# Kernel tuning notes

Measured on AMD Instinct MI355X. Metric: run time of the kernel, lower is better.

Reference implementation:

```python
import jax, jax.numpy as jnp
import numpy as np

QUERY_DIM = 1024
KEY_DIM = 1024
NUM_HEADS = 16
HEAD_DIM = QUERY_DIM // NUM_HEADS


def setup_inputs() -> dict:
    key = jax.random.key(0)
    ks = jax.random.split(key, 12)
    B, Sq, Sk = 2, 1024, 4096

    def xavier(k, fan_in, fan_out):
        limit = np.sqrt(6.0 / (fan_in + fan_out))
        return jax.random.uniform(k, (fan_in, fan_out), jnp.float32, -limit, limit)

    return {
        "query": jax.random.normal(ks[0], (B, Sq, QUERY_DIM), jnp.float32),
        "key": jax.random.normal(ks[1], (B, Sk, KEY_DIM), jnp.float32),
        "value": jax.random.normal(ks[2], (B, Sk, KEY_DIM), jnp.float32),
        "key_mask": jax.random.randint(ks[3], (B, Sk), 0, 2, jnp.int32),
        # projection weights stored as [in, out] for x @ W
        "Wq": xavier(ks[4], QUERY_DIM, NUM_HEADS * HEAD_DIM),
        "bq": jnp.zeros((NUM_HEADS * HEAD_DIM,), jnp.float32),
        "Wk": xavier(ks[5], KEY_DIM, NUM_HEADS * HEAD_DIM),
        "bk": jnp.zeros((NUM_HEADS * HEAD_DIM,), jnp.float32),
        "Wv": xavier(ks[6], KEY_DIM, NUM_HEADS * HEAD_DIM),
        "bv": jnp.zeros((NUM_HEADS * HEAD_DIM,), jnp.float32),
        "Wo": xavier(ks[7], NUM_HEADS * HEAD_DIM, QUERY_DIM),
        "bo": jnp.zeros((QUERY_DIM,), jnp.float32),
    }


def reference(query, key, value, key_mask, Wq, bq, Wk, bk, Wv, bv, Wo, bo):
    B, Sq, _ = query.shape
    Sk = key.shape[1]
    H, D = NUM_HEADS, HEAD_DIM
    scale = 1.0 / np.sqrt(D)

    q = (query @ Wq + bq).reshape(B, Sq, H, D)   # [B,Sq,H,D]
    k = (key @ Wk + bk).reshape(B, Sk, H, D)     # [B,Sk,H,D]
    v = (value @ Wv + bv).reshape(B, Sk, H, D)

    # scores: [B,H,Sq,Sk]
    scores = jnp.einsum("bqhd,bkhd->bhqk", q, k) * scale
    mask = (key_mask == 0)[:, None, None, :]  # [B,1,1,Sk]
    scores = jnp.where(mask, jnp.float32(-1e9), scores)
    probs = jax.nn.softmax(scores, axis=-1)
    # dropout is identity at eval (p effectively 0)
    ctx = jnp.einsum("bhqk,bkhd->bqhd", probs, v).reshape(B, Sq, H * D)
    return ctx @ Wo + bo
```

## Files before the change

### kernel.cpp

```cpp
#include <hip/hip_runtime.h>
#include <stdint.h>

#define NH 16
#define HD 64
#define SQ 1024
#define SK 4096
#define DM 1024
#define MQ 2048
#define MK 8192
#define MTOT 18432

typedef short s16x8 __attribute__((ext_vector_type(8)));
typedef float f32x4 __attribute__((ext_vector_type(4)));

#define GLOAD_LDS16(g, l) __builtin_amdgcn_global_load_lds( \
    (const __attribute__((address_space(1))) void*)(g), \
    (__attribute__((address_space(3))) void*)(l), 16, 0, 0)

__device__ __forceinline__ short f2bf(float f) {
  union { float f; uint32_t u; } v; v.f = f;
  uint32_t r = (v.u + 0x7FFFu + ((v.u >> 16) & 1u)) >> 16;
  return (short)(uint16_t)r;
}
__device__ __forceinline__ short f2bf_rz(float f) {
  union { float f; uint32_t u; } v; v.f = f;
  return (short)(uint16_t)(v.u >> 16);
}

__global__ void cvt_kernel(const float* __restrict__ src, short* __restrict__ dst, int n8) {
  int stride = gridDim.x * blockDim.x;
  for (int i = blockIdx.x * blockDim.x + threadIdx.x; i < n8; i += stride) {
    const float4* s4 = (const float4*)src + 2 * (size_t)i;
    float4 a = s4[0], b = s4[1];
    s16x8 o;
    o[0] = f2bf(a.x); o[1] = f2bf(a.y); o[2] = f2bf(a.z); o[3] = f2bf(a.w);
    o[4] = f2bf(b.x); o[5] = f2bf(b.y); o[6] = f2bf(b.z); o[7] = f2bf(b.w);
    *((s16x8*)dst + i) = o;
  }
}

__global__ void twkernel(const float* __restrict__ W, short* __restrict__ Wt) {
  __shared__ __align__(16) short t[64][65];
  int lx = threadIdx.x & 63, ly = threadIdx.x >> 6;
  int c0 = (blockIdx.x & 15) * 64, r0 = (blockIdx.x >> 4) * 64;
  #pragma unroll
  for (int i = ly; i < 64; i += 4) t[i][lx] = f2bf(W[(size_t)(r0 + i) * DM + c0 + lx]);
  __syncthreads();
  #pragma unroll
  for (int i = ly; i < 64; i += 4) Wt[(size_t)(c0 + i) * DM + r0 + lx] = t[lx][i];
}

__global__ __launch_bounds__(256) void proj_gemm(
    const short* __restrict__ Acat,
    const short* __restrict__ Wqt, const short* __restrict__ Wkt, const short* __restrict__ Wvt,
    const float* __restrict__ bq, const float* __restrict__ bk, const float* __restrict__ bv,
    short* __restrict__ Qp, short* __restrict__ Kp, short* __restrict__ Vp)
{
  __shared__ __align__(16) short As[128 * 32];
  __shared__ __align__(16) short Bs[128 * 32];
  int tid = threadIdx.x, lane = tid & 63, wid = tid >> 6;
  int bm = blockIdx.x >> 3, bn = blockIdx.x & 7;
  int m0 = bm * 128, n0 = bn * 128;
  int seg = (m0 < MQ) ? 0 : (m0 < MQ + MK) ? 1 : 2;
  const short* Wt = (seg == 0) ? Wqt : (seg == 1) ? Wkt : Wvt;
  const float* bias = (seg == 0) ? bq : (seg == 1) ? bk : bv;

  int off = tid * 16;
  int arow = off >> 6;
  int acol = (off & 63) >> 1;
  int wr = wid >> 1, wc = wid & 1;
  int l15 = lane & 15, g = lane >> 4, lh8 = g * 8;

  f32x4 acc[4][4] = {};

  const short* gA0 = Acat + (size_t)(m0 + arow) * DM + acol;
  const short* gA1 = Acat + (size_t)(m0 + arow + 64) * DM + acol;
  const short* gB0 = Wt + (size_t)(n0 + arow) * DM + acol;
  const short* gB1 = Wt + (size_t)(n0 + arow + 64) * DM + acol;

  for (int kt = 0; kt < 32; ++kt) {
    int k0 = kt * 32;
    __syncthreads();
    GLOAD_LDS16(gA0 + k0, (char*)As + off);
    GLOAD_LDS16(gA1 + k0, (char*)As + off + 4096);
    GLOAD_LDS16(gB0 + k0, (char*)Bs + off);
    GLOAD_LDS16(gB1 + k0, (char*)Bs + off + 4096);
    __syncthreads();
    s16x8 af[4], bfr[4];
    #pragma unroll
    for (int mi = 0; mi < 4; ++mi)
      af[mi] = *(const s16x8*)((const char*)As + ((wr * 64 + mi * 16 + l15) * 32 + lh8) * 2);
    #pragma unroll
    for (int ni = 0; ni < 4; ++ni)
      bfr[ni] = *(const s16x8*)((const char*)Bs + ((wc * 64 + ni * 16 + l15) * 32 + lh8) * 2);
    #pragma unroll
    for (int mi = 0; mi < 4; ++mi)
      #pragma unroll
      for (int ni = 0; ni < 4; ++ni)
        acc[mi][ni] = __builtin_amdgcn_mfma_f32_16x16x32_bf16(af[mi], bfr[ni], acc[mi][ni], 0, 0, 0);
  }

  __syncthreads();

  if (seg == 2) {
    short* tw = (short*)As + wid * 288;
    int vbase = m0 - (MQ + MK) + wr * 64;
    #pragma unroll
    for (int mi = 0; mi < 4; ++mi) {
      int vr = vbase + mi * 16 + l15;
      int bb2 = vr >> 12, sk = vr & 4095;
      #pragma unroll
      for (int ni = 0; ni < 4; ++ni) {
        int col = n0 + wc * 64 + ni * 16;
        int h = col >> 6, d0 = col & 63;
        float bb = bias[col + l15];
        #pragma unroll
        for (int r = 0; r < 4; ++r)
          tw[(g * 4 + r) * 18 + l15] = f2bf(acc[mi][ni][r] + bb);
        #pragma unroll
        for (int j = 0; j < 4; ++j) {
          int dl = g * 4 + j;
          Vp[((size_t)(bb2 * NH + h) * HD + d0 + dl) * SK + sk] = tw[l15 * 18 + dl];
        }
      }
    }
  } else {
    #pragma unroll
    for (int mi = 0; mi < 4; ++mi) {
      #pragma unroll
      for (int ni = 0; ni < 4; ++ni) {
        int col = n0 + wc * 64 + ni * 16 + l15;
        int h = col >> 6, d = col & 63;
        float bb = bias[col];
        #pragma unroll
        for (int r = 0; r < 4; ++r) {
          int row = m0 + wr * 64 + mi * 16 + g * 4 + r;
          short v16 = f2bf(acc[mi][ni][r] + bb);
          if (seg == 0) {
            int b = row >> 10, sq = row & 1023;
            Qp[((size_t)(b * NH + h) * SQ + sq) * HD + d] = v16;
          } else {
            int kr = row - MQ; int b = kr >> 12, sk = kr & 4095;
            Kp[((size_t)(b * NH + h) * SK + sk) * HD + d] = v16;
          }
        }
      }
    }
  }
}

__global__ __launch_bounds__(256) void attn_kernel(
    const short* __restrict__ Qp, const short* __restrict__ Kp, const short* __restrict__ Vp,
    const int* __restrict__ kmask, short* __restrict__ ctx)
{
  __shared__ __align__(16) short Ks[64 * 64];
  __shared__ __align__(16) short Vs[64 * 64];
  __shared__ __align__(16) short Ps[4][16 * 64];
  __shared__ float madd[SK];

  int tid = threadIdx.x, lane = tid & 63, wid = tid >> 6;
  int bh = blockIdx.x & 31, qt = blockIdx.x >> 5;
  int b = bh >> 4, h = bh & 15;
  const short* Qb = Qp + (size_t)bh * SQ * HD;
  const short* Kb = Kp + (size_t)bh * SK * HD;
  const short* Vb = Vp + (size_t)bh * HD * SK;
  const int* kmb = kmask + b * SK;

  for (int i = tid; i < SK; i += 256) madd[i] = kmb[i] ? 0.0f : -1e9f;

  int l15 = lane & 15, g = lane >> 4, lh8 = g * 8;
  int q0 = qt * 64 + wid * 16;
  int swz = (l15 & 7) << 4;

  s16x8 aq[2];
  aq[0] = *(const s16x8*)(Qb + (size_t)(q0 + l15) * HD + lh8);
  aq[1] = *(const s16x8*)(Qb + (size_t)(q0 + l15) * HD + 32 + lh8);

  f32x4 o[4] = {};
  float m_run[4], l_run[4];
  #pragma unroll
  for (int r = 0; r < 4; ++r) { m_run[r] = -3.0e38f; l_run[r] = 0.0f; }

  int srow = tid >> 3, scEl = (tid & 7) * 8;
  int wsoff = srow * 128 + ((scEl * 2) ^ ((srow & 7) << 4));

  s16x8 rk0, rk1, rv0, rv1;
#define ALOADS(t) { \
    rk0 = *(const s16x8*)(Kb + (size_t)((t) * 64 + srow) * HD + scEl); \
    rk1 = *(const s16x8*)(Kb + (size_t)((t) * 64 + srow + 32) * HD + scEl); \
    rv0 = *(const s16x8*)(Vb + (size_t)srow * SK + (t) * 64 + scEl); \
    rv1 = *(const s16x8*)(Vb + (size_t)(srow + 32) * SK + (t) * 64 + scEl); }

  ALOADS(0);
  const float sscale = 0.18033688f;
  for (int t = 0; t < 64; ++t) {
    __syncthreads();
    *(s16x8*)((char*)Ks + wsoff) = rk0;
    *(s16x8*)((char*)Ks + wsoff + 4096) = rk1;
    *(s16x8*)((char*)Vs + wsoff) = rv0;
    *(s16x8*)((char*)Vs + wsoff + 4096) = rv1;
    __syncthreads();
    if (t < 63) ALOADS(t + 1);

    f32x4 sc[4] = {};
    #pragma unroll
    for (int ni = 0; ni < 4; ++ni) {
      #pragma unroll
      for (int ks = 0; ks < 2; ++ks) {
        s16x8 kf = *(const s16x8*)((const char*)Ks + (ni * 16 + l15) * 128 + ((ks * 64 + g * 16) ^ swz));
        sc[ni] = __builtin_amdgcn_mfma_f32_16x16x32_bf16(aq[ks], kf, sc[ni], 0, 0, 0);
      }
    }
    #pragma unroll
    for (int ni = 0; ni < 4; ++ni) {
      float ma = madd[t * 64 + ni * 16 + l15];
      #pragma unroll
      for (int r = 0; r < 4; ++r) sc[ni][r] = sc[ni][r] * sscale + ma;
    }
    float alpha[4];
    #pragma unroll
    for (int r = 0; r < 4; ++r) {
      float pm = fmaxf(fmaxf(sc[0][r], sc[1][r]), fmaxf(sc[2][r], sc[3][r]));
      pm = fmaxf(pm, __shfl_xor(pm, 1));
      pm = fmaxf(pm, __shfl_xor(pm, 2));
      pm = fmaxf(pm, __shfl_xor(pm, 4));
      pm = fmaxf(pm, __shfl_xor(pm, 8));
      float mn = fmaxf(m_run[r], pm);
      alpha[r] = exp2f(m_run[r] - mn);
      m_run[r] = mn;
      float rs = 0.f;
      #pragma unroll
      for (int ni = 0; ni < 4; ++ni) { float p = exp2f(sc[ni][r] - mn); sc[ni][r] = p; rs += p; }
      rs += __shfl_xor(rs, 1);
      rs += __shfl_xor(rs, 2);
      rs += __shfl_xor(rs, 4);
      rs += __shfl_xor(rs, 8);
      l_run[r] = l_run[r] * alpha[r] + rs;
    }
    #pragma unroll
    for (int nd = 0; nd < 4; ++nd)
      #pragma unroll
      for (int r = 0; r < 4; ++r) o[nd][r] *= alpha[r];

    char* PsW = (char*)&Ps[wid][0];
    #pragma unroll
    for (int ni = 0; ni < 4; ++ni) {
      #pragma unroll
      for (int r = 0; r < 4; ++r) {
        int prow = g * 4 + r;
        *(short*)(PsW + prow * 128 + (((ni * 16 + l15) * 2) ^ ((prow & 7) << 4))) = f2bf_rz(sc[ni][r]);
      }
    }
    #pragma unroll
    for (int ks2 = 0; ks2 < 2; ++ks2) {
      s16x8 pa = *(const s16x8*)(PsW + l15 * 128 + ((ks2 * 64 + g * 16) ^ swz));
      #pragma unroll
      for (int nd = 0; nd < 4; ++nd) {
        s16x8 vf = *(const s16x8*)((const char*)Vs + (nd * 16 + l15) * 128 + ((ks2 * 64 + g * 16) ^ swz));
        o[nd] = __builtin_amdgcn_mfma_f32_16x16x32_bf16(pa, vf, o[nd], 0, 0, 0);
      }
    }
  }
#undef ALOADS

  #pragma unroll
  for (int nd = 0; nd < 4; ++nd) {
    #pragma unroll
    for (int r = 0; r < 4; ++r) {
      int q = q0 + g * 4 + r;
      int d = nd * 16 + l15;
      float val = o[nd][r] / l_run[r];
      ctx[((size_t)(b * SQ + q)) * DM + h * HD + d] = f2bf(val);
    }
  }
}

__global__ __launch_bounds__(256) void out_gemm(
    const short* __restrict__ Actx, const short* __restrict__ Wot,
    const float* __restrict__ bo, float* __restrict__ out)
{
  __shared__ __align__(16) short As[128 * 32];
  __shared__ __align__(16) short Bs[128 * 32];
  int tid = threadIdx.x, lane = tid & 63, wid = tid >> 6;
  int bm = blockIdx.x >> 3, bn = blockIdx.x & 7;
  int m0 = bm * 128, n0 = bn * 128;

  int off = tid * 16;
  int arow = off >> 6;
  int acol = (off & 63) >> 1;
  int wr = wid >> 1, wc = wid & 1;
  int l15 = lane & 15, lh8 = (lane >> 4) * 8;

  f32x4 acc[4][4] = {};

  const short* gA0 = Actx + (size_t)(m0 + arow) * DM + acol;
  const short* gA1 = Actx + (size_t)(m0 + arow + 64) * DM + acol;
  const short* gB0 = Wot + (size_t)(n0 + arow) * DM + acol;
  const short* gB1 = Wot + (size_t)(n0 + arow + 64) * DM + acol;

  for (int kt = 0; kt < 32; ++kt) {
    int k0 = kt * 32;
    __syncthreads();
    GLOAD_LDS16(gA0 + k0, (char*)As + off);
    GLOAD_LDS16(gA1 + k0, (char*)As + off + 4096);
    GLOAD_LDS16(gB0 + k0, (char*)Bs + off);
    GLOAD_LDS16(gB1 + k0, (char*)Bs + off + 4096);
    __syncthreads();
    s16x8 af[4], bfr[4];
    #pragma unroll
    for (int mi = 0; mi < 4; ++mi)
      af[mi] = *(const s16x8*)((const char*)As + ((wr * 64 + mi * 16 + l15) * 32 + lh8) * 2);
    #pragma unroll
    for (int ni = 0; ni < 4; ++ni)
      bfr[ni] = *(const s16x8*)((const char*)Bs + ((wc * 64 + ni * 16 + l15) * 32 + lh8) * 2);
    #pragma unroll
    for (int mi = 0; mi < 4; ++mi)
      #pragma unroll
      for (int ni = 0; ni < 4; ++ni)
        acc[mi][ni] = __builtin_amdgcn_mfma_f32_16x16x32_bf16(af[mi], bfr[ni], acc[mi][ni], 0, 0, 0);
  }

  #pragma unroll
  for (int mi = 0; mi < 4; ++mi) {
    #pragma unroll
    for (int ni = 0; ni < 4; ++ni) {
      int col = n0 + wc * 64 + ni * 16 + l15;
      float bb = bo[col];
      #pragma unroll
      for (int r = 0; r < 4; ++r) {
        int row = m0 + wr * 64 + mi * 16 + (lane >> 4) * 4 + r;
        out[(size_t)row * DM + col] = acc[mi][ni][r] + bb;
      }
    }
  }
}

extern "C" void kernel_launch(void* const* d_in, const int* in_sizes, int n_in,
                              void* d_out, int out_size, void* d_ws, size_t ws_size,
                              hipStream_t stream) {
  const float* query = (const float*)d_in[0];
  const float* key   = (const float*)d_in[1];
  const float* value = (const float*)d_in[2];
  const int*   kmask = (const int*)d_in[3];
  const float* Wq = (const float*)d_in[4];
  const float* bq = (const float*)d_in[5];
  const float* Wk = (const float*)d_in[6];
  const float* bk = (const float*)d_in[7];
  const float* Wv = (const float*)d_in[8];
  const float* bv = (const float*)d_in[9];
  const float* Wo = (const float*)d_in[10];
  const float* bo = (const float*)d_in[11];
  float* out = (float*)d_out;

  char* ws = (char*)d_ws;
  short* Acat = (short*)ws;
  short* Wqt  = (short*)(ws + (size_t)37748736);
  short* Wkt  = Wqt + 1048576;
  short* Wvt  = Wkt + 1048576;
  short* Wot  = Wvt + 1048576;
  short* Qp   = Wot + 1048576;
  short* Kp   = Qp + 2097152;
  short* Vp   = Kp + 8388608;
  short* ctx  = Vp + 8388608;

  short* qbf = Acat;
  short* kbf = Acat + 2097152;
  short* vbf = Acat + 2097152 + 8388608;

  cvt_kernel<<<1024, 256, 0, stream>>>(query, qbf, 2097152 / 8);
  cvt_kernel<<<2048, 256, 0, stream>>>(key,   kbf, 8388608 / 8);
  cvt_kernel<<<2048, 256, 0, stream>>>(value, vbf, 8388608 / 8);
  twkernel<<<256, 256, 0, stream>>>(Wq, Wqt);
  twkernel<<<256, 256, 0, stream>>>(Wk, Wkt);
  twkernel<<<256, 256, 0, stream>>>(Wv, Wvt);
  twkernel<<<256, 256, 0, stream>>>(Wo, Wot);
  proj_gemm<<<1152, 256, 0, stream>>>(Acat, Wqt, Wkt, Wvt, bq, bk, bv, Qp, Kp, Vp);
  attn_kernel<<<512, 256, 0, stream>>>(Qp, Kp, Vp, kmask, ctx);
  out_gemm<<<128, 256, 0, stream>>>(ctx, Wot, bo, out);
}
```

Measured before the change: 380.3 us.

## Double-buffer K/V tiles, lazy rescale, and MFMA row-sum in attention loop

Double-buffers the K and V shared-memory tiles so staging the next tile overlaps compute, which cuts the per-iteration barriers from two to one. The online softmax now skips rescaling unless the max grows by more than a threshold (8 in log2 units), and the row-sum is computed with an extra MFMA against a ones vector instead of shuffle reductions. s_setprio hints are added around the MFMA blocks. The cost is more LDS use, which may lower occupancy, and a row-sum built from bf16-rounded probabilities.

```diff
diff --git a/kernel.cpp b/kernel.cpp
--- a/kernel.cpp
+++ b/kernel.cpp
@@ -153,8 +153,8 @@
     const short* __restrict__ Qp, const short* __restrict__ Kp, const short* __restrict__ Vp,
     const int* __restrict__ kmask, short* __restrict__ ctx)
 {
-  __shared__ __align__(16) short Ks[64 * 64];
-  __shared__ __align__(16) short Vs[64 * 64];
+  __shared__ __align__(16) short Ks[2][64 * 64];
+  __shared__ __align__(16) short Vs[2][64 * 64];
   __shared__ __align__(16) short Ps[4][16 * 64];
   __shared__ float madd[SK];
 
@@ -176,10 +176,15 @@
   aq[0] = *(const s16x8*)(Qb + (size_t)(q0 + l15) * HD + lh8);
   aq[1] = *(const s16x8*)(Qb + (size_t)(q0 + l15) * HD + 32 + lh8);
 
+  s16x8 ones;
+  #pragma unroll
+  for (int j = 0; j < 8; ++j) ones[j] = (short)0x3F80;
+
   f32x4 o[4] = {};
-  float m_run[4], l_run[4];
-  #pragma unroll
-  for (int r = 0; r < 4; ++r) { m_run[r] = -3.0e38f; l_run[r] = 0.0f; }
+  f32x4 ol = {};
+  float m_run[4];
+  #pragma unroll
+  for (int r = 0; r < 4; ++r) m_run[r] = -3.0e38f;
 
   int srow = tid >> 3, scEl = (tid & 7) * 8;
   int wsoff = srow * 128 + ((scEl * 2) ^ ((srow & 7) << 4));
@@ -190,78 +195,93 @@
     rk1 = *(const s16x8*)(Kb + (size_t)((t) * 64 + srow + 32) * HD + scEl); \
     rv0 = *(const s16x8*)(Vb + (size_t)srow * SK + (t) * 64 + scEl); \
     rv1 = *(const s16x8*)(Vb + (size_t)(srow + 32) * SK + (t) * 64 + scEl); }
-
-  ALOADS(0);
+#define STAGE(bi) { \
+    char* kb_ = (char*)Ks[bi]; char* vb_ = (char*)Vs[bi]; \
+    *(s16x8*)(kb_ + wsoff) = rk0; *(s16x8*)(kb_ + wsoff + 4096) = rk1; \
+    *(s16x8*)(vb_ + wsoff) = rv0; *(s16x8*)(vb_ + wsoff + 4096) = rv1; }
+
+  ALOADS(0); STAGE(0); ALOADS(1);
+  __syncthreads();
+
   const float sscale = 0.18033688f;
   for (int t = 0; t < 64; ++t) {
-    __syncthreads();
-    *(s16x8*)((char*)Ks + wsoff) = rk0;
-    *(s16x8*)((char*)Ks + wsoff + 4096) = rk1;
-    *(s16x8*)((char*)Vs + wsoff) = rv0;
-    *(s16x8*)((char*)Vs + wsoff + 4096) = rv1;
-    __syncthreads();
-    if (t < 63) ALOADS(t + 1);
+    int cur = t & 1;
+    if (t < 63) STAGE(cur ^ 1);
+    if (t < 62) ALOADS(t + 2);
+    const char* KsB = (const char*)Ks[cur];
+    const char* VsB = (const char*)Vs[cur];
 
     f32x4 sc[4] = {};
+    __builtin_amdgcn_s_setprio(1);
     #pragma unroll
     for (int ni = 0; ni < 4; ++ni) {
       #pragma unroll
       for (int ks = 0; ks < 2; ++ks) {
-        s16x8 kf = *(const s16x8*)((const char*)Ks + (ni * 16 + l15) * 128 + ((ks * 64 + g * 16) ^ swz));
+        s16x8 kf = *(const s16x8*)(KsB + (ni * 16 + l15) * 128 + ((ks * 64 + g * 16) ^ swz));
         sc[ni] = __builtin_amdgcn_mfma_f32_16x16x32_bf16(aq[ks], kf, sc[ni], 0, 0, 0);
       }
     }
+    __builtin_amdgcn_s_setprio(0);
+
     #pragma unroll
     for (int ni = 0; ni < 4; ++ni) {
       float ma = madd[t * 64 + ni * 16 + l15];
       #pragma unroll
       for (int r = 0; r < 4; ++r) sc[ni][r] = sc[ni][r] * sscale + ma;
     }
-    float alpha[4];
+
+    float pm[4];
+    int upd = 0;
     #pragma unroll
     for (int r = 0; r < 4; ++r) {
-      float pm = fmaxf(fmaxf(sc[0][r], sc[1][r]), fmaxf(sc[2][r], sc[3][r]));
-      pm = fmaxf(pm, __shfl_xor(pm, 1));
-      pm = fmaxf(pm, __shfl_xor(pm, 2));
-      pm = fmaxf(pm, __shfl_xor(pm, 4));
-      pm = fmaxf(pm, __shfl_xor(pm, 8));
-      float mn = fmaxf(m_run[r], pm);
-      alpha[r] = exp2f(m_run[r] - mn);
-      m_run[r] = mn;
-      float rs = 0.f;
-      #pragma unroll
-      for (int ni = 0; ni < 4; ++ni) { float p = exp2f(sc[ni][r] - mn); sc[ni][r] = p; rs += p; }
-      rs += __shfl_xor(rs, 1);
-      rs += __shfl_xor(rs, 2);
-      rs += __shfl_xor(rs, 4);
-      rs += __shfl_xor(rs, 8);
-      l_run[r] = l_run[r] * alpha[r] + rs;
-    }
-    #pragma unroll
-    for (int nd = 0; nd < 4; ++nd)
-      #pragma unroll
-      for (int r = 0; r < 4; ++r) o[nd][r] *= alpha[r];
+      float p = fmaxf(fmaxf(sc[0][r], sc[1][r]), fmaxf(sc[2][r], sc[3][r]));
+      p = fmaxf(p, __shfl_xor(p, 1));
+      p = fmaxf(p, __shfl_xor(p, 2));
+      p = fmaxf(p, __shfl_xor(p, 4));
+      p = fmaxf(p, __shfl_xor(p, 8));
+      pm[r] = p;
+      upd |= (p > m_run[r] + 8.0f);
+    }
+    if (__any(upd)) {
+      #pragma unroll
+      for (int r = 0; r < 4; ++r) {
+        float mn = fmaxf(m_run[r], pm[r]);
+        float alpha = exp2f(m_run[r] - mn);
+        m_run[r] = mn;
+        #pragma unroll
+        for (int nd = 0; nd < 4; ++nd) o[nd][r] *= alpha;
+        ol[r] *= alpha;
+      }
+    }
 
     char* PsW = (char*)&Ps[wid][0];
     #pragma unroll
     for (int ni = 0; ni < 4; ++ni) {
       #pragma unroll
       for (int r = 0; r < 4; ++r) {
+        float p = exp2f(sc[ni][r] - m_run[r]);
         int prow = g * 4 + r;
-        *(short*)(PsW + prow * 128 + (((ni * 16 + l15) * 2) ^ ((prow & 7) << 4))) = f2bf_rz(sc[ni][r]);
-      }
-    }
+        *(short*)(PsW + prow * 128 + (((ni * 16 + l15) * 2) ^ ((prow & 7) << 4))) = f2bf_rz(p);
+      }
+    }
+    asm volatile("s_waitcnt lgkmcnt(0)" ::: "memory");
+
+    __builtin_amdgcn_s_setprio(1);
     #pragma unroll
     for (int ks2 = 0; ks2 < 2; ++ks2) {
       s16x8 pa = *(const s16x8*)(PsW + l15 * 128 + ((ks2 * 64 + g * 16) ^ swz));
       #pragma unroll
       for (int nd = 0; nd < 4; ++nd) {
-        s16x8 vf = *(const s16x8*)((const char*)Vs + (nd * 16 + l15) * 128 + ((ks2 * 64 + g * 16) ^ swz));
+        s16x8 vf = *(const s16x8*)(VsB + (nd * 16 + l15) * 128 + ((ks2 * 64 + g * 16) ^ swz));
         o[nd] = __builtin_amdgcn_mfma_f32_16x16x32_bf16(pa, vf, o[nd], 0, 0, 0);
       }
-    }
+      ol = __builtin_amdgcn_mfma_f32_16x16x32_bf16(pa, ones, ol, 0, 0, 0);
+    }
+    __builtin_amdgcn_s_setprio(0);
+    __syncthreads();
   }
 #undef ALOADS
+#undef STAGE
 
   #pragma unroll
   for (int nd = 0; nd < 4; ++nd) {
@@ -269,7 +289,7 @@
     for (int r = 0; r < 4; ++r) {
       int q = q0 + g * 4 + r;
       int d = nd * 16 + l15;
-      float val = o[nd][r] / l_run[r];
+      float val = o[nd][r] / ol[r];
       ctx[((size_t)(b * SQ + q)) * DM + h * HD + d] = f2bf(val);
     }
   }
```

New measurement: 355.4 us. 1.07x faster.
